# Optimization experiments

Measured on AMD Instinct MI355X. Metric: run time of the kernel, lower is better.

## Reference

```python
import jax, jax.numpy as jnp
import numpy as np
from functools import partial

B, L, D = 4, 1024, 512
H = 8                 # attention heads
DIN = 2 * D           # mamba d_inner (expand=2)
N = 16                # mamba d_state
K = 4                 # mamba d_conv
R = 32                # dt_rank = ceil(D/16)


def setup_inputs() -> dict:
    key = jax.random.key(0)
    ks = jax.random.split(key, 24)
    s = 0.02
    nrm = lambda k, sh: (jax.random.normal(k, sh, dtype=jnp.float32) * s)
    inp = {
        'x':       jax.random.normal(ks[0], (B, L, D), dtype=jnp.float32),
        # attention projections
        'Wq': nrm(ks[1], (D, D)), 'bq': jnp.zeros((D,), jnp.float32),
        'Wk': nrm(ks[2], (D, D)), 'bk': jnp.zeros((D,), jnp.float32),
        'Wv': nrm(ks[3], (D, D)), 'bv': jnp.zeros((D,), jnp.float32),
        'Wo': nrm(ks[4], (D, D)), 'bo': jnp.zeros((D,), jnp.float32),
        # layernorms
        'ln1_g': jnp.ones((D,), jnp.float32), 'ln1_b': jnp.zeros((D,), jnp.float32),
        'ln2_g': jnp.ones((D,), jnp.float32), 'ln2_b': jnp.zeros((D,), jnp.float32),
        # mamba params
        'm_Win':   nrm(ks[5], (D, 2 * DIN)),            # in_proj (no bias)
        'm_conv_w': nrm(ks[6], (DIN, 1, K)),            # depthwise causal conv
        'm_conv_b': jnp.zeros((DIN,), jnp.float32),
        'm_Wx':    nrm(ks[7], (DIN, R + 2 * N)),        # x_proj (no bias)
        'm_Wdt':   nrm(ks[8], (R, DIN)),                # dt_proj
        'm_bdt':   jnp.full((DIN,), 0.5, jnp.float32),
        'm_Alog':  jnp.log(jnp.broadcast_to(jnp.arange(1, N + 1, dtype=jnp.float32), (DIN, N))).copy(),
        'm_D':     jnp.ones((DIN,), jnp.float32),
        'm_Wout':  nrm(ks[9], (DIN, D)),                # out_proj (no bias)
    }
    return inp


def _layernorm(x, g, b, eps=1e-5):
    mu = jnp.mean(x, axis=-1, keepdims=True)
    var = jnp.var(x, axis=-1, keepdims=True)
    return (x - mu) * jax.lax.rsqrt(var + eps) * g + b


def _mamba(x, Win, conv_w, conv_b, Wx, Wdt, bdt, Alog, Dp, Wout):
    b, l, _ = x.shape
    xz = x @ Win                           # [B,L,2*DIN]
    xi, z = xz[..., :DIN], xz[..., DIN:]
    # causal depthwise conv over time
    xt = jnp.transpose(xi, (0, 2, 1))      # [B,DIN,L]
    xt = jax.lax.conv_general_dilated(
        xt, conv_w, window_strides=(1,), padding=[(K - 1, 0)],
        feature_group_count=DIN, dimension_numbers=('NCH', 'OIH', 'NCH'))
    xc = jax.nn.silu(jnp.transpose(xt, (0, 2, 1)) + conv_b)   # [B,L,DIN]
    # input-dependent SSM params
    dbl = xc @ Wx                          # [B,L,R+2N]
    dt = jax.nn.softplus(dbl[..., :R] @ Wdt + bdt)            # [B,L,DIN]
    Bm = dbl[..., R:R + N]                 # [B,L,N]
    Cm = dbl[..., R + N:]                  # [B,L,N]
    A = -jnp.exp(Alog)                     # [DIN,N]
    dA = jnp.exp(dt[..., None] * A)                     # [B,L,DIN,N]
    dBx = (dt * xc)[..., None] * Bm[:, :, None, :]      # [B,L,DIN,N]

    def step(h, t):
        dA_t, dBx_t, C_t = t
        h = h * dA_t + dBx_t               # [B,DIN,N]
        y = jnp.einsum('bdn,bn->bd', h, C_t)
        return h, y

    h0 = jnp.zeros((b, DIN, N), xc.dtype)
    _, ys = jax.lax.scan(step, h0, (jnp.swapaxes(dA, 0, 1),
                                    jnp.swapaxes(dBx, 0, 1),
                                    jnp.swapaxes(Cm, 0, 1)))
    y = jnp.swapaxes(ys, 0, 1)             # [B,L,DIN]
    y = y + xc * Dp
    y = y * jax.nn.silu(z)
    return y @ Wout                        # [B,L,D]


def reference(x, Wq, bq, Wk, bk, Wv, bv, Wo, bo, ln1_g, ln1_b, ln2_g, ln2_b,
              m_Win, m_conv_w, m_conv_b, m_Wx, m_Wdt, m_bdt, m_Alog, m_D, m_Wout):
    b, l, d = x.shape
    E = d // H
    q = (x @ Wq + bq).reshape(b, l, H, E)
    k = (x @ Wk + bk).reshape(b, l, H, E)
    v = (x @ Wv + bv).reshape(b, l, H, E)
    scores = jnp.einsum('blhe,bshe->bhls', q, k) * (E ** -0.5)
    attn = jax.nn.softmax(scores, axis=-1)                    # [B,H,L,L]
    o = jnp.einsum('bhls,bshe->blhe', attn, v).reshape(b, l, d)
    new_x = o @ Wo + bo
    x1 = _layernorm(x + new_x, ln1_g, ln1_b)
    y = _mamba(x1, m_Win, m_conv_w, m_conv_b, m_Wx, m_Wdt, m_bdt, m_Alog, m_D, m_Wout)
    out = _layernorm(x1 + y, ln2_g, ln2_b)
    return out, attn
```

## Files before the change

### kernel.cpp

```cpp
#include <hip/hip_runtime.h>
#include <hip/hip_bf16.h>

#define BB 4
#define LL 1024
#define DD 512
#define HH 8
#define EE 64
#define DIN 1024
#define NN 16
#define KK 4
#define RR 32
#define BL (BB*LL)
#define CC 16
#define LC (LL/CC)
#define BDN (BB*DIN*NN)

using bf16 = __hip_bfloat16;
typedef __attribute__((ext_vector_type(8))) short short8;
typedef __attribute__((ext_vector_type(4))) float f32x4;

__device__ __forceinline__ float ldf(const float* p) { return *p; }
__device__ __forceinline__ float ldf(const bf16* p) { return __bfloat162float(*p); }
__device__ __forceinline__ void stf(float* p, float v) { *p = v; }
__device__ __forceinline__ void stf(bf16* p, float v) { *p = __float2bfloat16(v); }
__device__ __forceinline__ short f2bs(float f) { bf16 h = __float2bfloat16(f); return *(short*)&h; }

__global__ void cvt_k(const float* __restrict__ in, bf16* __restrict__ out, int n)
{
    int i = blockIdx.x * 256 + threadIdx.x;
    if (i < n) out[i] = __float2bfloat16(in[i]);
}

__global__ void tpw_k(const float* __restrict__ in, bf16* __restrict__ outT,
                      int Kd, int Nd)
{
    __shared__ float t[32][33];
    const int n0 = blockIdx.x * 32, k0 = blockIdx.y * 32;
    const int tx = threadIdx.x & 31, ty = threadIdx.x >> 5;
#pragma unroll
    for (int i = 0; i < 4; ++i)
        t[ty + 8 * i][tx] = in[(size_t)(k0 + ty + 8 * i) * Nd + n0 + tx];
    __syncthreads();
#pragma unroll
    for (int i = 0; i < 4; ++i)
        outT[(size_t)(n0 + ty + 8 * i) * Kd + k0 + tx] = __float2bfloat16(t[tx][ty + 8 * i]);
}

__global__ void tpv_k(const bf16* __restrict__ v, bf16* __restrict__ vT)
{
    __shared__ float t[32][33];
    const int l0 = blockIdx.x * 32;
    const int e0 = blockIdx.y * 32;
    const int bh = blockIdx.z, b = bh >> 3, h = bh & 7;
    const int tx = threadIdx.x & 31, ty = threadIdx.x >> 5;
#pragma unroll
    for (int i = 0; i < 4; ++i)
        t[ty + 8 * i][tx] = ldf(&v[(size_t)(b * LL + l0 + ty + 8 * i) * DD + h * EE + e0 + tx]);
    __syncthreads();
#pragma unroll
    for (int i = 0; i < 4; ++i)
        stf(&vT[(size_t)(bh * EE + e0 + ty + 8 * i) * LL + l0 + tx], t[tx][ty + 8 * i]);
}

template <typename TC>
__global__ void mfma_gemm_k(const bf16* __restrict__ A, int lda,
                            const bf16* __restrict__ Bt, int ldb,
                            const float* __restrict__ bias,
                            TC* __restrict__ C, int ldc, int Kd)
{
    const int lane = threadIdx.x & 63;
    const int w = threadIdx.x >> 6;
    const int m = lane & 15, quad = lane >> 4;
    const int m0 = blockIdx.y * 64 + (w >> 1) * 32;
    const int n0 = blockIdx.x * 64 + (w & 1) * 32;
    f32x4 acc[2][2] = {};
    const bf16* a0p = A + (size_t)(m0 + m) * lda + quad * 8;
    const bf16* a1p = a0p + (size_t)16 * lda;
    const bf16* b0p = Bt + (size_t)(n0 + m) * ldb + quad * 8;
    const bf16* b1p = b0p + (size_t)16 * ldb;
    for (int k = 0; k < Kd; k += 32) {
        short8 a0 = *(const short8*)(a0p + k);
        short8 a1 = *(const short8*)(a1p + k);
        short8 b0 = *(const short8*)(b0p + k);
        short8 b1 = *(const short8*)(b1p + k);
        acc[0][0] = __builtin_amdgcn_mfma_f32_16x16x32_bf16(a0, b0, acc[0][0], 0, 0, 0);
        acc[0][1] = __builtin_amdgcn_mfma_f32_16x16x32_bf16(a0, b1, acc[0][1], 0, 0, 0);
        acc[1][0] = __builtin_amdgcn_mfma_f32_16x16x32_bf16(a1, b0, acc[1][0], 0, 0, 0);
        acc[1][1] = __builtin_amdgcn_mfma_f32_16x16x32_bf16(a1, b1, acc[1][1], 0, 0, 0);
    }
#pragma unroll
    for (int i = 0; i < 2; ++i)
#pragma unroll
        for (int j = 0; j < 2; ++j)
#pragma unroll
            for (int r = 0; r < 4; ++r) {
                int row = m0 + i * 16 + quad * 4 + r;
                int col = n0 + j * 16 + (lane & 15);
                float vv = acc[i][j][r] + (bias ? bias[col] : 0.f);
                stf(&C[(size_t)row * ldc + col], vv);
            }
}

__global__ void attn_fused_k(const bf16* __restrict__ q, const bf16* __restrict__ k,
                             const bf16* __restrict__ vT,
                             float* __restrict__ attn, bf16* __restrict__ o)
{
    const int rt = blockIdx.x;
    const int bh = blockIdx.y, b = bh >> 3, h = bh & 7;
    const int w = threadIdx.x >> 6;
    const int lane = threadIdx.x & 63;
    const int m = lane & 15, quad = lane >> 4;
    __shared__ float pm[4][16], ps[4][16];
    __shared__ bf16 P[16][1032];

    const bf16* qp = q + (size_t)(b * LL + rt * 16 + m) * DD + h * EE + quad * 8;
    short8 a0 = *(const short8*)(qp);
    short8 a1 = *(const short8*)(qp + 32);

    f32x4 acc[16];
#pragma unroll
    for (int t = 0; t < 16; ++t) {
        int srow = w * 256 + t * 16 + m;
        const bf16* kp = k + (size_t)(b * LL + srow) * DD + h * EE + quad * 8;
        short8 b0 = *(const short8*)(kp);
        short8 b1 = *(const short8*)(kp + 32);
        f32x4 c = {};
        c = __builtin_amdgcn_mfma_f32_16x16x32_bf16(a0, b0, c, 0, 0, 0);
        c = __builtin_amdgcn_mfma_f32_16x16x32_bf16(a1, b1, c, 0, 0, 0);
        acc[t] = c;
    }

#pragma unroll
    for (int r = 0; r < 4; ++r) {
        float mx = -1e30f;
#pragma unroll
        for (int t = 0; t < 16; ++t) { acc[t][r] *= 0.125f; mx = fmaxf(mx, acc[t][r]); }
        mx = fmaxf(mx, __shfl_xor(mx, 1)); mx = fmaxf(mx, __shfl_xor(mx, 2));
        mx = fmaxf(mx, __shfl_xor(mx, 4)); mx = fmaxf(mx, __shfl_xor(mx, 8));
        if (m == 0) pm[w][quad * 4 + r] = mx;
    }
    __syncthreads();
#pragma unroll
    for (int r = 0; r < 4; ++r) {
        float mx = fmaxf(fmaxf(pm[0][quad * 4 + r], pm[1][quad * 4 + r]),
                         fmaxf(pm[2][quad * 4 + r], pm[3][quad * 4 + r]));
        float s = 0.f;
#pragma unroll
        for (int t = 0; t < 16; ++t) { float e = __expf(acc[t][r] - mx); acc[t][r] = e; s += e; }
        s += __shfl_xor(s, 1); s += __shfl_xor(s, 2);
        s += __shfl_xor(s, 4); s += __shfl_xor(s, 8);
        if (m == 0) ps[w][quad * 4 + r] = s;
    }
    __syncthreads();
#pragma unroll
    for (int r = 0; r < 4; ++r) {
        float tot = ps[0][quad * 4 + r] + ps[1][quad * 4 + r] + ps[2][quad * 4 + r] + ps[3][quad * 4 + r];
        float inv = 1.f / tot;
        int row = rt * 16 + quad * 4 + r;
        float* op = attn + ((size_t)bh * LL + row) * LL + w * 256 + (lane & 15);
#pragma unroll
        for (int t = 0; t < 16; ++t) {
            float pv = acc[t][r] * inv;
            op[t * 16] = pv;
            P[quad * 4 + r][w * 256 + t * 16 + m] = __float2bfloat16(pv);
        }
    }
    __syncthreads();

    const bf16* vp = vT + (size_t)(bh * EE + w * 16 + m) * LL + quad * 8;
    f32x4 oacc = {};
    for (int k0 = 0; k0 < LL; k0 += 32) {
        short8 af = *(const short8*)(&P[m][k0 + quad * 8]);
        short8 bf = *(const short8*)(vp + k0);
        oacc = __builtin_amdgcn_mfma_f32_16x16x32_bf16(af, bf, oacc, 0, 0, 0);
    }
#pragma unroll
    for (int r = 0; r < 4; ++r) {
        int row = rt * 16 + quad * 4 + r;
        stf(&o[(size_t)(b * LL + row) * DD + h * EE + w * 16 + (lane & 15)], oacc[r]);
    }
}

template <typename TA, typename TC>
__global__ void gemm_k(const TA* __restrict__ A, int lda,
                       const float* __restrict__ B, int ldb,
                       const float* __restrict__ bias,
                       TC* __restrict__ C, int ldc,
                       int M, int N, int Kd)
{
    __shared__ float As[32][33];
    __shared__ float Bs[32][33];
    const int tid = threadIdx.x;
    const int tx = tid & 31;
    const int ty = tid >> 5;
    const int rowBase = blockIdx.y * 32;
    const int colBase = blockIdx.x * 32;
    float acc[4] = {0.f, 0.f, 0.f, 0.f};

    for (int k0 = 0; k0 < Kd; k0 += 32) {
#pragma unroll
        for (int i = 0; i < 4; ++i) {
            int r = ty + 8 * i;
            As[r][tx] = ldf(&A[(size_t)(rowBase + r) * lda + k0 + tx]);
            Bs[r][tx] = B[(size_t)(k0 + r) * ldb + colBase + tx];
        }
        __syncthreads();
#pragma unroll 8
        for (int kk = 0; kk < 32; ++kk) {
            float bv = Bs[kk][tx];
#pragma unroll
            for (int i = 0; i < 4; ++i) acc[i] += As[ty + 8 * i][kk] * bv;
        }
        __syncthreads();
    }
#pragma unroll
    for (int i = 0; i < 4; ++i) {
        int row = rowBase + ty + 8 * i;
        int col = colBase + tx;
        float r = acc[i] + (bias ? bias[col] : 0.f);
        stf(&C[(size_t)row * ldc + col], r);
    }
}

template <typename TA, typename TR, typename TO>
__global__ void add_ln_k(const TA* __restrict__ a, const TR* __restrict__ r,
                         const float* __restrict__ g, const float* __restrict__ be,
                         TO* __restrict__ out)
{
    const int row = blockIdx.x;
    const int tid = threadIdx.x;
    __shared__ float red[256];
    const size_t base = (size_t)row * DD;
    float v0 = ldf(&a[base + tid]) + ldf(&r[base + tid]);
    float v1 = ldf(&a[base + 256 + tid]) + ldf(&r[base + 256 + tid]);
    red[tid] = v0 + v1;
    __syncthreads();
    for (int off = 128; off > 0; off >>= 1) {
        if (tid < off) red[tid] += red[tid + off];
        __syncthreads();
    }
    const float mu = red[0] * (1.f / 512.f);
    __syncthreads();
    float d0 = v0 - mu, d1 = v1 - mu;
    red[tid] = d0 * d0 + d1 * d1;
    __syncthreads();
    for (int off = 128; off > 0; off >>= 1) {
        if (tid < off) red[tid] += red[tid + off];
        __syncthreads();
    }
    const float rs = rsqrtf(red[0] * (1.f / 512.f) + 1e-5f);
    stf(&out[base + tid], d0 * rs * g[tid] + be[tid]);
    stf(&out[base + 256 + tid], d1 * rs * g[tid + 256] + be[tid + 256]);
}

__global__ void conv_silu_k(const bf16* __restrict__ xz,
                            const float* __restrict__ w,
                            const float* __restrict__ cb,
                            bf16* __restrict__ xc)
{
    const int idx = blockIdx.x * 256 + threadIdx.x;
    const int c = idx & (DIN - 1);
    const int t = (idx >> 10) & (LL - 1);
    const int b = idx >> 20;
    float acc = cb[c];
    const bf16* xi = xz + (size_t)b * LL * (2 * DIN) + c;
#pragma unroll
    for (int j = 0; j < KK; ++j) {
        int tt = t - (KK - 1) + j;
        if (tt >= 0) acc += w[c * KK + j] * ldf(&xi[(size_t)tt * (2 * DIN)]);
    }
    stf(&xc[idx], acc / (1.f + __expf(-acc)));
}

__global__ void softplus_k(bf16* __restrict__ p)
{
    const int idx = blockIdx.x * 256 + threadIdx.x;
    float v = ldf(&p[idx]);
    stf(&p[idx], (v > 20.f) ? v : log1pf(__expf(v)));
}

__global__ void scan_p1_k(const bf16* __restrict__ dt, const bf16* __restrict__ xc,
                          const float* __restrict__ dbl, const float* __restrict__ Alog,
                          float* __restrict__ P, float* __restrict__ S)
{
    const int tid = threadIdx.x;
    const int n = tid & (NN - 1);
    const int dl = tid >> 4;
    const int c = blockIdx.x & (CC - 1);
    const int d = (blockIdx.x >> 4) * 16 + dl;
    const int b = blockIdx.y;
    const float A = -__expf(Alog[d * NN + n]);
    const int t0 = c * LC;
    const bf16* dt_b = dt + ((size_t)b * LL + t0) * DIN + d;
    const bf16* xc_b = xc + ((size_t)b * LL + t0) * DIN + d;
    const float* dbl_b = dbl + ((size_t)b * LL + t0) * 64;
    float Pv = 1.f, Sv = 0.f;
    for (int t = 0; t < LC; ++t) {
        float dtv = ldf(&dt_b[(size_t)t * DIN]);
        float xcv = ldf(&xc_b[(size_t)t * DIN]);
        float Bm = dbl_b[(size_t)t * 64 + RR + n];
        float dA = __expf(dtv * A);
        Sv = Sv * dA + dtv * xcv * Bm;
        Pv *= dA;
    }
    const size_t bdn = ((size_t)(b * DIN + d)) * NN + n;
    P[(size_t)c * BDN + bdn] = Pv;
    S[(size_t)c * BDN + bdn] = Sv;
}

__global__ void scan_p2_k(const float* __restrict__ P, const float* __restrict__ S,
                          float* __restrict__ Hc)
{
    const size_t bdn = (size_t)blockIdx.x * 256 + threadIdx.x;
    float h = 0.f;
#pragma unroll
    for (int c = 0; c < CC; ++c) {
        Hc[(size_t)c * BDN + bdn] = h;
        h = S[(size_t)c * BDN + bdn] + P[(size_t)c * BDN + bdn] * h;
    }
}

__global__ void scan_p3_k(const bf16* __restrict__ dt, const bf16* __restrict__ xc,
                          const float* __restrict__ dbl, const float* __restrict__ Alog,
                          const float* __restrict__ Dv, const float* __restrict__ Hc,
                          bf16* __restrict__ xzm)
{
    const int tid = threadIdx.x;
    const int n = tid & (NN - 1);
    const int dl = tid >> 4;
    const int c = blockIdx.x & (CC - 1);
    const int d = (blockIdx.x >> 4) * 16 + dl;
    const int b = blockIdx.y;
    const float A = -__expf(Alog[d * NN + n]);
    const float Dp = Dv[d];
    const int t0 = c * LC;
    const bf16* dt_b = dt + ((size_t)b * LL + t0) * DIN + d;
    const bf16* xc_b = xc + ((size_t)b * LL + t0) * DIN + d;
    const float* dbl_b = dbl + ((size_t)b * LL + t0) * 64;
    bf16* xz_b = xzm + ((size_t)b * LL + t0) * (2 * DIN);
    const size_t bdn = ((size_t)(b * DIN + d)) * NN + n;
    float h = Hc[(size_t)c * BDN + bdn];
    for (int t = 0; t < LC; ++t) {
        float dtv = ldf(&dt_b[(size_t)t * DIN]);
        float xcv = ldf(&xc_b[(size_t)t * DIN]);
        float Bm = dbl_b[(size_t)t * 64 + RR + n];
        float Cm = dbl_b[(size_t)t * 64 + RR + NN + n];
        h = h * __expf(dtv * A) + dtv * xcv * Bm;
        float p = h * Cm;
        p += __shfl_xor(p, 1);
        p += __shfl_xor(p, 2);
        p += __shfl_xor(p, 4);
        p += __shfl_xor(p, 8);
        if (n == 0) {
            float zv = ldf(&xz_b[(size_t)t * (2 * DIN) + DIN + d]);
            float yv = p + xcv * Dp;
            yv *= zv / (1.f + __expf(-zv));
            stf(&xz_b[(size_t)t * (2 * DIN) + d], yv);
        }
    }
}

extern "C" void kernel_launch(void* const* d_in, const int* in_sizes, int n_in,
                              void* d_out, int out_size, void* d_ws, size_t ws_size,
                              hipStream_t stream)
{
    const float* x    = (const float*)d_in[0];
    const float* Wq   = (const float*)d_in[1];
    const float* bq   = (const float*)d_in[2];
    const float* Wk   = (const float*)d_in[3];
    const float* bk   = (const float*)d_in[4];
    const float* Wv   = (const float*)d_in[5];
    const float* bv   = (const float*)d_in[6];
    const float* Wo   = (const float*)d_in[7];
    const float* bo   = (const float*)d_in[8];
    const float* g1   = (const float*)d_in[9];
    const float* b1   = (const float*)d_in[10];
    const float* g2   = (const float*)d_in[11];
    const float* b2   = (const float*)d_in[12];
    const float* Win  = (const float*)d_in[13];
    const float* cw   = (const float*)d_in[14];
    const float* cb   = (const float*)d_in[15];
    const float* Wx   = (const float*)d_in[16];
    const float* Wdt  = (const float*)d_in[17];
    const float* bdt  = (const float*)d_in[18];
    const float* Alog = (const float*)d_in[19];
    const float* Dv   = (const float*)d_in[20];
    const float* Wout = (const float*)d_in[21];

    float* out  = (float*)d_out;
    float* attn = out + (size_t)BL * DD;

    const size_t M1 = 1048576;
    bf16* wsb = (bf16*)d_ws;
    bf16* xb   = wsb;
    bf16* q    = wsb + 2*M1;
    bf16* kb   = wsb + 4*M1;
    bf16* v    = wsb + 6*M1;
    bf16* o    = wsb + 8*M1;
    bf16* x1   = wsb + 10*M1;
    bf16* xz   = wsb + 12*M1;
    bf16* xc   = wsb + 20*M1;
    bf16* dtb  = wsb + 24*M1;
    float* dbl = (float*)(wsb + 28*M1);
    bf16* vT   = wsb + 28*M1 + 524288;
    bf16* Wqt  = vT + 2*M1;
    bf16* Wkt  = Wqt + 262144;
    bf16* Wvt  = Wkt + 262144;
    bf16* Wot  = Wvt + 262144;
    bf16* Wint = Wot + 262144;
    bf16* Wxt  = Wint + M1;
    bf16* Woutt= Wxt + 65536;
    bf16* newx = q;
    bf16* ym   = v;
    float* Pp = (float*)xb;
    float* Sp = (float*)q;
    float* Hc = (float*)o;

    const dim3 blk(256);

    cvt_k<<<dim3(BL*DD/256), blk, 0, stream>>>(x, xb, BL*DD);
    tpw_k<<<dim3(DD/32, DD/32),  blk, 0, stream>>>(Wq,   Wqt,  DD, DD);
    tpw_k<<<dim3(DD/32, DD/32),  blk, 0, stream>>>(Wk,   Wkt,  DD, DD);
    tpw_k<<<dim3(DD/32, DD/32),  blk, 0, stream>>>(Wv,   Wvt,  DD, DD);
    tpw_k<<<dim3(DD/32, DD/32),  blk, 0, stream>>>(Wo,   Wot,  DD, DD);
    tpw_k<<<dim3(2*DIN/32, DD/32), blk, 0, stream>>>(Win, Wint, DD, 2*DIN);
    tpw_k<<<dim3(64/32, DIN/32), blk, 0, stream>>>(Wx,   Wxt,  DIN, 64);
    tpw_k<<<dim3(DD/32, DIN/32), blk, 0, stream>>>(Wout, Woutt, DIN, DD);

    mfma_gemm_k<bf16><<<dim3(DD/64, BL/64), blk, 0, stream>>>(xb, DD, Wqt, DD, bq, q,  DD, DD);
    mfma_gemm_k<bf16><<<dim3(DD/64, BL/64), blk, 0, stream>>>(xb, DD, Wkt, DD, bk, kb, DD, DD);
    mfma_gemm_k<bf16><<<dim3(DD/64, BL/64), blk, 0, stream>>>(xb, DD, Wvt, DD, bv, v,  DD, DD);
    tpv_k<<<dim3(LL/32, EE/32, BB*HH), blk, 0, stream>>>(v, vT);

    attn_fused_k<<<dim3(LL/16, BB*HH), blk, 0, stream>>>(q, kb, vT, attn, o);

    mfma_gemm_k<bf16><<<dim3(DD/64, BL/64), blk, 0, stream>>>(o, DD, Wot, DD, bo, newx, DD, DD);
    add_ln_k<float, bf16, bf16><<<dim3(BL), blk, 0, stream>>>(x, newx, g1, b1, x1);

    mfma_gemm_k<bf16><<<dim3(2*DIN/64, BL/64), blk, 0, stream>>>(x1, DD, Wint, DD, nullptr, xz, 2*DIN, DD);

    conv_silu_k<<<dim3(BL*DIN/256), blk, 0, stream>>>(xz, cw, cb, xc);

    mfma_gemm_k<float><<<dim3(64/64, BL/64), blk, 0, stream>>>(xc, DIN, Wxt, DIN, nullptr, dbl, 64, DIN);

    gemm_k<float, bf16><<<dim3(DIN/32, BL/32), blk, 0, stream>>>(dbl, 64, Wdt, DIN, bdt, dtb, DIN, BL, DIN, RR);
    softplus_k<<<dim3(BL*DIN/256), blk, 0, stream>>>(dtb);

    scan_p1_k<<<dim3((DIN/16)*CC, BB), blk, 0, stream>>>(dtb, xc, dbl, Alog, Pp, Sp);
    scan_p2_k<<<dim3(BDN/256), blk, 0, stream>>>(Pp, Sp, Hc);
    scan_p3_k<<<dim3((DIN/16)*CC, BB), blk, 0, stream>>>(dtb, xc, dbl, Alog, Dv, Hc, xz);

    mfma_gemm_k<bf16><<<dim3(DD/64, BL/64), blk, 0, stream>>>(xz, 2*DIN, Woutt, DIN, nullptr, ym, DD, DIN);

    add_ln_k<bf16, bf16, float><<<dim3(BL), blk, 0, stream>>>(x1, ym, g2, b2, out);
}
```

Before: 640.9 us.

## Restructure selective scan to one thread per channel and fuse softplus into dt GEMM

The chunked scan now gives each thread one channel with all 16 state elements in registers. This removes the per-timestep shuffle reduction across 16 lanes and the redundant dt/xc loads per state element. The chunk count doubles to keep enough blocks, and chunk decay P is computed as exp(sum(dt)*A) instead of a running product. Softplus moves into the dt-projection GEMM epilogue, which removes a separate elementwise pass over the dt buffer. The scan workspace buffers are reassigned so the larger P/S/Hc arrays fit. The trade-off is higher register pressure and fewer threads per block-row, with B/C loads now scalar broadcasts.

```diff
diff --git a/kernel.cpp b/kernel.cpp
--- a/kernel.cpp
+++ b/kernel.cpp
@@ -11,7 +11,7 @@
 #define KK 4
 #define RR 32
 #define BL (BB*LL)
-#define CC 16
+#define CC 32
 #define LC (LL/CC)
 #define BDN (BB*DIN*NN)
 
@@ -181,7 +181,7 @@
     }
 }
 
-template <typename TA, typename TC>
+template <typename TA, typename TC, bool SP>
 __global__ void gemm_k(const TA* __restrict__ A, int lda,
                        const float* __restrict__ B, int ldb,
                        const float* __restrict__ bias,
@@ -218,6 +218,7 @@
         int row = rowBase + ty + 8 * i;
         int col = colBase + tx;
         float r = acc[i] + (bias ? bias[col] : 0.f);
+        if (SP) r = (r > 20.f) ? r : log1pf(__expf(r));
         stf(&C[(size_t)row * ldc + col], r);
     }
 }
@@ -272,40 +273,40 @@
     stf(&xc[idx], acc / (1.f + __expf(-acc)));
 }
 
-__global__ void softplus_k(bf16* __restrict__ p)
-{
-    const int idx = blockIdx.x * 256 + threadIdx.x;
-    float v = ldf(&p[idx]);
-    stf(&p[idx], (v > 20.f) ? v : log1pf(__expf(v)));
-}
-
 __global__ void scan_p1_k(const bf16* __restrict__ dt, const bf16* __restrict__ xc,
                           const float* __restrict__ dbl, const float* __restrict__ Alog,
                           float* __restrict__ P, float* __restrict__ S)
 {
-    const int tid = threadIdx.x;
-    const int n = tid & (NN - 1);
-    const int dl = tid >> 4;
-    const int c = blockIdx.x & (CC - 1);
-    const int d = (blockIdx.x >> 4) * 16 + dl;
+    const int d = (blockIdx.x & 3) * 256 + threadIdx.x;
+    const int c = blockIdx.x >> 2;
     const int b = blockIdx.y;
-    const float A = -__expf(Alog[d * NN + n]);
+    float A[NN];
+#pragma unroll
+    for (int n = 0; n < NN; ++n) A[n] = -__expf(Alog[d * NN + n]);
     const int t0 = c * LC;
     const bf16* dt_b = dt + ((size_t)b * LL + t0) * DIN + d;
     const bf16* xc_b = xc + ((size_t)b * LL + t0) * DIN + d;
-    const float* dbl_b = dbl + ((size_t)b * LL + t0) * 64;
-    float Pv = 1.f, Sv = 0.f;
+    const float* dbl_b = dbl + ((size_t)b * LL + t0) * 64 + RR;
+    float h[NN];
+#pragma unroll
+    for (int n = 0; n < NN; ++n) h[n] = 0.f;
+    float sdt = 0.f;
+#pragma unroll 4
     for (int t = 0; t < LC; ++t) {
         float dtv = ldf(&dt_b[(size_t)t * DIN]);
         float xcv = ldf(&xc_b[(size_t)t * DIN]);
-        float Bm = dbl_b[(size_t)t * 64 + RR + n];
-        float dA = __expf(dtv * A);
-        Sv = Sv * dA + dtv * xcv * Bm;
-        Pv *= dA;
-    }
-    const size_t bdn = ((size_t)(b * DIN + d)) * NN + n;
-    P[(size_t)c * BDN + bdn] = Pv;
-    S[(size_t)c * BDN + bdn] = Sv;
+        float dtx = dtv * xcv;
+        sdt += dtv;
+#pragma unroll
+        for (int n = 0; n < NN; ++n) {
+            float dA = __expf(dtv * A[n]);
+            h[n] = h[n] * dA + dtx * dbl_b[(size_t)t * 64 + n];
+        }
+    }
+    float* Pp = P + (size_t)c * BDN + ((size_t)(b * DIN + d)) * NN;
+    float* Sp = S + (size_t)c * BDN + ((size_t)(b * DIN + d)) * NN;
+#pragma unroll
+    for (int n = 0; n < NN; ++n) { Pp[n] = __expf(sdt * A[n]); Sp[n] = h[n]; }
 }
 
 __global__ void scan_p2_k(const float* __restrict__ P, const float* __restrict__ S,
@@ -325,38 +326,38 @@
                           const float* __restrict__ Dv, const float* __restrict__ Hc,
                           bf16* __restrict__ xzm)
 {
-    const int tid = threadIdx.x;
-    const int n = tid & (NN - 1);
-    const int dl = tid >> 4;
-    const int c = blockIdx.x & (CC - 1);
-    const int d = (blockIdx.x >> 4) * 16 + dl;
+    const int d = (blockIdx.x & 3) * 256 + threadIdx.x;
+    const int c = blockIdx.x >> 2;
     const int b = blockIdx.y;
-    const float A = -__expf(Alog[d * NN + n]);
+    float A[NN];
+#pragma unroll
+    for (int n = 0; n < NN; ++n) A[n] = -__expf(Alog[d * NN + n]);
     const float Dp = Dv[d];
     const int t0 = c * LC;
     const bf16* dt_b = dt + ((size_t)b * LL + t0) * DIN + d;
     const bf16* xc_b = xc + ((size_t)b * LL + t0) * DIN + d;
-    const float* dbl_b = dbl + ((size_t)b * LL + t0) * 64;
+    const float* dbl_b = dbl + ((size_t)b * LL + t0) * 64 + RR;
     bf16* xz_b = xzm + ((size_t)b * LL + t0) * (2 * DIN);
-    const size_t bdn = ((size_t)(b * DIN + d)) * NN + n;
-    float h = Hc[(size_t)c * BDN + bdn];
+    const float* hp = Hc + (size_t)c * BDN + ((size_t)(b * DIN + d)) * NN;
+    float h[NN];
+#pragma unroll
+    for (int n = 0; n < NN; ++n) h[n] = hp[n];
+#pragma unroll 2
     for (int t = 0; t < LC; ++t) {
         float dtv = ldf(&dt_b[(size_t)t * DIN]);
         float xcv = ldf(&xc_b[(size_t)t * DIN]);
-        float Bm = dbl_b[(size_t)t * 64 + RR + n];
-        float Cm = dbl_b[(size_t)t * 64 + RR + NN + n];
-        h = h * __expf(dtv * A) + dtv * xcv * Bm;
-        float p = h * Cm;
-        p += __shfl_xor(p, 1);
-        p += __shfl_xor(p, 2);
-        p += __shfl_xor(p, 4);
-        p += __shfl_xor(p, 8);
-        if (n == 0) {
-            float zv = ldf(&xz_b[(size_t)t * (2 * DIN) + DIN + d]);
-            float yv = p + xcv * Dp;
-            yv *= zv / (1.f + __expf(-zv));
-            stf(&xz_b[(size_t)t * (2 * DIN) + d], yv);
+        float dtx = dtv * xcv;
+        float y = 0.f;
+#pragma unroll
+        for (int n = 0; n < NN; ++n) {
+            float dA = __expf(dtv * A[n]);
+            h[n] = h[n] * dA + dtx * dbl_b[(size_t)t * 64 + n];
+            y += h[n] * dbl_b[(size_t)t * 64 + NN + n];
         }
+        float zv = ldf(&xz_b[(size_t)t * (2 * DIN) + DIN + d]);
+        float yv = y + xcv * Dp;
+        yv *= zv / (1.f + __expf(-zv));
+        stf(&xz_b[(size_t)t * (2 * DIN) + d], yv);
     }
 }
 
@@ -413,8 +414,8 @@
     bf16* newx = q;
     bf16* ym   = v;
     float* Pp = (float*)xb;
-    float* Sp = (float*)q;
-    float* Hc = (float*)o;
+    float* Sp = (float*)kb;
+    float* Hc = (float*)vT;
 
     const dim3 blk(256);
 
@@ -443,12 +444,11 @@
 
     mfma_gemm_k<float><<<dim3(64/64, BL/64), blk, 0, stream>>>(xc, DIN, Wxt, DIN, nullptr, dbl, 64, DIN);
 
-    gemm_k<float, bf16><<<dim3(DIN/32, BL/32), blk, 0, stream>>>(dbl, 64, Wdt, DIN, bdt, dtb, DIN, BL, DIN, RR);
-    softplus_k<<<dim3(BL*DIN/256), blk, 0, stream>>>(dtb);
-
-    scan_p1_k<<<dim3((DIN/16)*CC, BB), blk, 0, stream>>>(dtb, xc, dbl, Alog, Pp, Sp);
+    gemm_k<float, bf16, true><<<dim3(DIN/32, BL/32), blk, 0, stream>>>(dbl, 64, Wdt, DIN, bdt, dtb, DIN, BL, DIN, RR);
+
+    scan_p1_k<<<dim3((DIN/256)*CC, BB), blk, 0, stream>>>(dtb, xc, dbl, Alog, Pp, Sp);
     scan_p2_k<<<dim3(BDN/256), blk, 0, stream>>>(Pp, Sp, Hc);
-    scan_p3_k<<<dim3((DIN/16)*CC, BB), blk, 0, stream>>>(dtb, xc, dbl, Alog, Dv, Hc, xz);
+    scan_p3_k<<<dim3((DIN/256)*CC, BB), blk, 0, stream>>>(dtb, xc, dbl, Alog, Dv, Hc, xz);
 
     mfma_gemm_k<bf16><<<dim3(DD/64, BL/64), blk, 0, stream>>>(xz, 2*DIN, Woutt, DIN, nullptr, ym, DD, DIN);
 
```

Measured after the change: 564.9 us. 11.9% less time.
